# Kernel tuning notes

Measured on AMD Instinct MI355X. Metric: run time of the kernel, lower is better.

Reference implementation:

```python
import jax, jax.numpy as jnp
import numpy as np

B, N, D, H = 4, 2048, 512, 8
HEAD = D // H
TEMP = 8.0


def setup_inputs() -> dict:
    key = jax.random.key(0)
    k1, k2, k3, k4 = jax.random.split(key, 4)
    return {
        "keys": jax.random.normal(k1, (B, N, D), dtype=jnp.float32),
        "queries": jax.random.normal(k2, (B, N, D), dtype=jnp.float32),
        "values": jax.random.normal(k3, (B, N, D), dtype=jnp.float32),
        "W_comb": jax.random.normal(k4, (D, D), dtype=jnp.float32) * (1.0 / np.sqrt(D)),
        "b_comb": jnp.zeros((D,), dtype=jnp.float32),
    }


def reference(keys, queries, values, W_comb, b_comb):
    b, nk, d = keys.shape
    nq = queries.shape[1]
    h, hd = H, HEAD
    # split heads: (b, n, d) -> (b, n, h, hd)
    k = keys.reshape(b, nk, h, hd)
    q = queries.reshape(b, nq, h, hd)
    v = values.reshape(b, nk, h, hd)
    # scaled dot-product attention per head
    logits = jnp.einsum("bqhd,bkhd->bhqk", q, k) / TEMP  # (b, h, nq, nk)
    w = jax.nn.softmax(logits, axis=-1)
    out = jnp.einsum("bhqk,bkhd->bqhd", w, v).reshape(b, nq, d)
    # head_combine: Linear with bias (torch: x @ W.T + b)
    return out @ W_comb.T + b_comb
```

## Files before the change

kernel.cpp:

```cpp
#include <hip/hip_runtime.h>

#define B_ 4
#define N_ 2048
#define D_ 512
#define H_ 8

typedef __attribute__((ext_vector_type(8))) short bf16x8;
typedef __attribute__((ext_vector_type(4))) short bf16x4;
typedef __attribute__((ext_vector_type(4))) float f32x4;

#define KP 68

__device__ __forceinline__ unsigned short f32_to_bf16(float f) {
  unsigned int u = __float_as_uint(f);
  u += 0x7FFFu + ((u >> 16) & 1u);
  return (unsigned short)(u >> 16);
}

__device__ __forceinline__ unsigned int pack2_bf16(float a, float b) {
  return (unsigned int)f32_to_bf16(a) | ((unsigned int)f32_to_bf16(b) << 16);
}

__device__ __forceinline__ bf16x8 cvt8_bf16(float4 a, float4 b, float s) {
  union { unsigned int u[4]; bf16x8 v; } r;
  r.u[0] = pack2_bf16(a.x * s, a.y * s);
  r.u[1] = pack2_bf16(a.z * s, a.w * s);
  r.u[2] = pack2_bf16(b.x * s, b.y * s);
  r.u[3] = pack2_bf16(b.z * s, b.w * s);
  return r.v;
}

__device__ __forceinline__ float fast_exp2(float x) {
#if __has_builtin(__builtin_amdgcn_exp2f)
  return __builtin_amdgcn_exp2f(x);
#else
  return exp2f(x);
#endif
}

__device__ __forceinline__ f32x4 mfma16(bf16x4 a, bf16x4 b, f32x4 c) {
#if __has_builtin(__builtin_amdgcn_mfma_f32_16x16x16_bf16)
  return __builtin_amdgcn_mfma_f32_16x16x16_bf16(a, b, c, 0, 0, 0);
#else
  return __builtin_amdgcn_mfma_f32_16x16x16bf16_1k(a, b, c, 0, 0, 0);
#endif
}

__global__ __launch_bounds__(256) void convert_kernel(
    const float* __restrict__ Kf, const float* __restrict__ Vf,
    unsigned short* __restrict__ Kb, unsigned short* __restrict__ Vt) {
  __shared__ float tile[64 * 72];
  const int tid = threadIdx.x;
  if (blockIdx.x < 1024) {
    int gid = blockIdx.x * 256 + tid;
    const float4* K4 = (const float4*)Kf;
    for (int i = gid; i < (B_ * N_ * D_) / 4; i += 262144) {
      float4 k = K4[i];
      ((uint2*)Kb)[i] = make_uint2(pack2_bf16(k.x, k.y), pack2_bf16(k.z, k.w));
    }
  } else {
    int bid = blockIdx.x - 1024;
    int nt = bid & 31, bh = bid >> 5;
    int b = bh >> 3, h = bh & 7;
    int n0 = nt * 64;
#pragma unroll
    for (int i = 0; i < 4; ++i) {
      int idx = i * 256 + tid;
      int r = idx >> 4, c = idx & 15;
      *(float4*)&tile[r * 72 + c * 4] =
          *(const float4*)(Vf + (size_t)(b * N_ + n0 + r) * D_ + h * 64 + c * 4);
    }
    __syncthreads();
    int d = tid >> 2, c = tid & 3;
    unsigned int o[8];
#pragma unroll
    for (int j = 0; j < 8; ++j)
      o[j] = pack2_bf16(tile[(c * 16 + 2 * j) * 72 + d],
                        tile[(c * 16 + 2 * j + 1) * 72 + d]);
    unsigned short* dst = Vt + ((size_t)bh * 64 + d) * N_ + n0 + c * 16;
    *(bf16x8*)dst = *(bf16x8*)&o[0];
    *(bf16x8*)(dst + 8) = *(bf16x8*)&o[4];
  }
}

__global__ __launch_bounds__(256, 2) void attn_kernel(
    const float* __restrict__ Qf, const unsigned short* __restrict__ Kb,
    const unsigned short* __restrict__ Vt, unsigned short* __restrict__ Ob) {
  __shared__ unsigned short Kl[2][64 * KP];
  __shared__ unsigned short Vl[2][64 * KP];

  const int tid = threadIdx.x;
  const int w = tid >> 6;
  const int lane = tid & 63;
  const int lr = lane & 15;
  const int lq = lane >> 4;

  const int lid = blockIdx.y * gridDim.x + blockIdx.x;
  const int xcd = lid & 7;
  const int lin = lid >> 3;
  const int bh = xcd * 4 + (lin >> 4);
  const int qb = (lin & 15) * 128;

  const size_t slab = (size_t)(bh >> 3) * N_ * D_ + (size_t)(bh & 7) * 64;
  const unsigned short* kbase = Kb + slab;
  const unsigned short* vtbase = Vt + (size_t)bh * 64 * N_;

  bf16x8 qa[2][2];
  {
    const float qs = 0.125f * 1.4426950408889634f;
#pragma unroll
    for (int g = 0; g < 2; ++g) {
      const float* qrow =
          Qf + slab + (size_t)(qb + w * 32 + g * 16 + lr) * D_;
      float4 a0 = *(const float4*)(qrow + 8 * lq);
      float4 a1 = *(const float4*)(qrow + 8 * lq + 4);
      qa[g][0] = cvt8_bf16(a0, a1, qs);
      float4 b0 = *(const float4*)(qrow + 32 + 8 * lq);
      float4 b1 = *(const float4*)(qrow + 36 + 8 * lq);
      qa[g][1] = cvt8_bf16(b0, b1, qs);
    }
  }

  f32x4 O[4][2];
#pragma unroll
  for (int i = 0; i < 4; ++i)
#pragma unroll
    for (int g = 0; g < 2; ++g) O[i][g] = (f32x4){0.f, 0.f, 0.f, 0.f};
  float l_g[2] = {0.f, 0.f};

  const int st_r = tid >> 3;
  const int st_c = tid & 7;

  {
    const unsigned short* ksrc = kbase + (size_t)st_r * D_ + st_c * 8;
    bf16x8 a = *(const bf16x8*)ksrc;
    bf16x8 b = *(const bf16x8*)(ksrc + (size_t)32 * D_);
    const unsigned short* vsrc = vtbase + (size_t)st_r * N_ + st_c * 8;
    bf16x8 c = *(const bf16x8*)vsrc;
    bf16x8 d = *(const bf16x8*)(vsrc + (size_t)32 * N_);
    *(bf16x8*)&Kl[0][st_r * KP + st_c * 8] = a;
    *(bf16x8*)&Kl[0][(st_r + 32) * KP + st_c * 8] = b;
    *(bf16x8*)&Vl[0][st_r * KP + st_c * 8] = c;
    *(bf16x8*)&Vl[0][(st_r + 32) * KP + st_c * 8] = d;
  }

  for (int kt = 0; kt < 32; ++kt) {
    const int p = kt & 1;
    __syncthreads();

    bf16x8 nk0, nk1, nv0, nv1;
    const bool more = (kt + 1) < 32;
    if (more) {
      const int kb1 = (kt + 1) * 64;
      const unsigned short* ksrc = kbase + (size_t)(kb1 + st_r) * D_ + st_c * 8;
      nk0 = *(const bf16x8*)ksrc;
      nk1 = *(const bf16x8*)(ksrc + (size_t)32 * D_);
      const unsigned short* vsrc = vtbase + (size_t)st_r * N_ + kb1 + st_c * 8;
      nv0 = *(const bf16x8*)vsrc;
      nv1 = *(const bf16x8*)(vsrc + (size_t)32 * N_);
    }

    f32x4 S[4][2];
#pragma unroll
    for (int nt = 0; nt < 4; ++nt) {
      bf16x8 kf0 = *(const bf16x8*)&Kl[p][(nt * 16 + lr) * KP + 8 * lq];
      bf16x8 kf1 = *(const bf16x8*)&Kl[p][(nt * 16 + lr) * KP + 32 + 8 * lq];
#pragma unroll
      for (int g = 0; g < 2; ++g) {
        S[nt][g] = __builtin_amdgcn_mfma_f32_16x16x32_bf16(
            kf0, qa[g][0], (f32x4){0.f, 0.f, 0.f, 0.f}, 0, 0, 0);
        S[nt][g] = __builtin_amdgcn_mfma_f32_16x16x32_bf16(kf1, qa[g][1],
                                                           S[nt][g], 0, 0, 0);
      }
    }

    bf16x4 pf[4][2];
#pragma unroll
    for (int nt = 0; nt < 4; ++nt)
#pragma unroll
      for (int g = 0; g < 2; ++g) {
        float p0 = fast_exp2(S[nt][g][0]);
        float p1 = fast_exp2(S[nt][g][1]);
        float p2 = fast_exp2(S[nt][g][2]);
        float p3 = fast_exp2(S[nt][g][3]);
        l_g[g] += (p0 + p1) + (p2 + p3);
        uint2 packed = make_uint2(pack2_bf16(p0, p1), pack2_bf16(p2, p3));
        pf[nt][g] = *(bf16x4*)&packed;
      }

#pragma unroll
    for (int dt = 0; dt < 4; ++dt) {
#pragma unroll
      for (int nt = 0; nt < 4; ++nt) {
        bf16x4 vf =
            *(const bf16x4*)&Vl[p][(dt * 16 + lr) * KP + nt * 16 + 4 * lq];
#pragma unroll
        for (int g = 0; g < 2; ++g)
          O[dt][g] = mfma16(vf, pf[nt][g], O[dt][g]);
      }
    }

    if (more) {
      *(bf16x8*)&Kl[1 - p][st_r * KP + st_c * 8] = nk0;
      *(bf16x8*)&Kl[1 - p][(st_r + 32) * KP + st_c * 8] = nk1;
      *(bf16x8*)&Vl[1 - p][st_r * KP + st_c * 8] = nv0;
      *(bf16x8*)&Vl[1 - p][(st_r + 32) * KP + st_c * 8] = nv1;
    }
  }

#pragma unroll
  for (int g = 0; g < 2; ++g) {
    l_g[g] += __shfl_xor(l_g[g], 16);
    l_g[g] += __shfl_xor(l_g[g], 32);
  }

  __syncthreads();
  unsigned short* SR = &Kl[0][0];
#pragma unroll
  for (int g = 0; g < 2; ++g) {
    float linv = 1.0f / l_g[g];
#pragma unroll
    for (int dt = 0; dt < 4; ++dt) {
      float v0 = O[dt][g][0] * linv;
      float v1 = O[dt][g][1] * linv;
      float v2 = O[dt][g][2] * linv;
      float v3 = O[dt][g][3] * linv;
      uint2 packed = make_uint2(pack2_bf16(v0, v1), pack2_bf16(v2, v3));
      *(bf16x4*)&SR[(w * 32 + g * 16 + lr) * KP + dt * 16 + lq * 4] =
          *(bf16x4*)&packed;
    }
  }
  __syncthreads();
  {
    const int row = tid >> 1, half = tid & 1;
    unsigned short* dst = Ob + slab + (size_t)(qb + row) * D_ + half * 32;
    const unsigned short* src = &SR[row * KP + half * 32];
    *(bf16x8*)dst = *(const bf16x8*)src;
    *(bf16x8*)(dst + 8) = *(const bf16x8*)(src + 8);
    *(bf16x8*)(dst + 16) = *(const bf16x8*)(src + 16);
    *(bf16x8*)(dst + 24) = *(const bf16x8*)(src + 24);
  }
}

#define GP 68
__global__ __launch_bounds__(256, 2) void gemm_kernel(
    const unsigned short* __restrict__ A, const float* __restrict__ Wf,
    const float* __restrict__ bias, float* __restrict__ out) {
  __shared__ unsigned short A_lds[2][64 * GP];
  __shared__ unsigned short W_lds[2][128 * GP];

  const int tid = threadIdx.x;
  const int w = tid >> 6;
  const int lane = tid & 63;
  const int lr = lane & 15;
  const int lq = lane >> 4;

  const int bid = blockIdx.x;
  const int xcd = bid & 7;
  const int lin = bid >> 3;
  const int mb = (xcd * 16 + (lin >> 2)) * 64;
  const int cb = (lin & 3) * 128;

  const int dc = (tid & 7) * 8;
  const int r0 = tid >> 3;

  f32x4 acc[8];
#pragma unroll
  for (int i = 0; i < 8; ++i) acc[i] = (f32x4){0.f, 0.f, 0.f, 0.f};

  {
    *(bf16x8*)&A_lds[0][r0 * GP + dc] =
        *(const bf16x8*)(A + (size_t)(mb + r0) * D_ + dc);
    *(bf16x8*)&A_lds[0][(r0 + 32) * GP + dc] =
        *(const bf16x8*)(A + (size_t)(mb + r0 + 32) * D_ + dc);
#pragma unroll
    for (int j = 0; j < 4; ++j) {
      const float* wsrc = Wf + (size_t)(cb + r0 + 32 * j) * D_ + dc;
      float4 wa = *(const float4*)wsrc;
      float4 wb = *(const float4*)(wsrc + 4);
      *(bf16x8*)&W_lds[0][(r0 + 32 * j) * GP + dc] = cvt8_bf16(wa, wb, 1.0f);
    }
  }

  for (int kt = 0; kt < 8; ++kt) {
    const int p = kt & 1;
    __syncthreads();

    bf16x8 na0, na1;
    float4 nwA[4], nwB[4];
    const bool more = (kt + 1) < 8;
    if (more) {
      const int k1 = (kt + 1) * 64;
      na0 = *(const bf16x8*)(A + (size_t)(mb + r0) * D_ + k1 + dc);
      na1 = *(const bf16x8*)(A + (size_t)(mb + r0 + 32) * D_ + k1 + dc);
#pragma unroll
      for (int j = 0; j < 4; ++j) {
        const float* wsrc = Wf + (size_t)(cb + r0 + 32 * j) * D_ + k1 + dc;
        nwA[j] = *(const float4*)wsrc;
        nwB[j] = *(const float4*)(wsrc + 4);
      }
    }

    bf16x8 a0 = *(const bf16x8*)&A_lds[p][(w * 16 + lr) * GP + 8 * lq];
    bf16x8 a1 = *(const bf16x8*)&A_lds[p][(w * 16 + lr) * GP + 32 + 8 * lq];
#pragma unroll
    for (int nt = 0; nt < 8; ++nt) {
      bf16x8 b0 = *(const bf16x8*)&W_lds[p][(nt * 16 + lr) * GP + 8 * lq];
      bf16x8 b1 = *(const bf16x8*)&W_lds[p][(nt * 16 + lr) * GP + 32 + 8 * lq];
      acc[nt] = __builtin_amdgcn_mfma_f32_16x16x32_bf16(a0, b0, acc[nt], 0, 0, 0);
      acc[nt] = __builtin_amdgcn_mfma_f32_16x16x32_bf16(a1, b1, acc[nt], 0, 0, 0);
    }

    if (more) {
      *(bf16x8*)&A_lds[1 - p][r0 * GP + dc] = na0;
      *(bf16x8*)&A_lds[1 - p][(r0 + 32) * GP + dc] = na1;
#pragma unroll
      for (int j = 0; j < 4; ++j)
        *(bf16x8*)&W_lds[1 - p][(r0 + 32 * j) * GP + dc] =
            cvt8_bf16(nwA[j], nwB[j], 1.0f);
    }
  }

#pragma unroll
  for (int nt = 0; nt < 8; ++nt) {
    float bc = bias[cb + nt * 16 + lr];
#pragma unroll
    for (int rr = 0; rr < 4; ++rr) {
      int row = mb + w * 16 + lq * 4 + rr;
      out[(size_t)row * D_ + cb + nt * 16 + lr] = acc[nt][rr] + bc;
    }
  }
}

extern "C" void kernel_launch(void* const* d_in, const int* in_sizes, int n_in,
                              void* d_out, int out_size, void* d_ws,
                              size_t ws_size, hipStream_t stream) {
  (void)in_sizes; (void)n_in; (void)out_size; (void)ws_size;
  const float* keys    = (const float*)d_in[0];
  const float* queries = (const float*)d_in[1];
  const float* values  = (const float*)d_in[2];
  const float* W       = (const float*)d_in[3];
  const float* bias    = (const float*)d_in[4];
  float* out = (float*)d_out;

  char* ws = (char*)d_ws;
  unsigned short* Kb = (unsigned short*)(ws + 8388608);
  unsigned short* Vt = (unsigned short*)(ws + 16777216);
  unsigned short* Ab = (unsigned short*)(ws + 25690112);

  convert_kernel<<<2048, 256, 0, stream>>>(keys, values, Kb, Vt);

  attn_kernel<<<dim3(N_ / 128, B_ * H_), 256, 0, stream>>>(queries, Kb, Vt, Ab);

  gemm_kernel<<<512, 256, 0, stream>>>(Ab, W, bias, out);
}
```

Baseline: 163.7 us.

## Fuse convert, attention and projection into one persistent kernel with grid barriers

Merges the three separate launches (K/V bf16 conversion, attention, head-combine GEMM) into a single 512-block kernel that separates the phases with software grid-wide barriers built on atomic counters, which are reset by a memset before each launch. The aim is to remove the launch gaps and tail effects between kernels. In exchange it adds a memset, atomic spin-wait barriers, and the requirement that all 512 blocks be co-resident. Fewer blocks now do the convert phase than before.

```diff
diff --git a/kernel.cpp b/kernel.cpp
--- a/kernel.cpp
+++ b/kernel.cpp
@@ -4,12 +4,14 @@
 #define N_ 2048
 #define D_ 512
 #define H_ 8
+#define NBLK 512
 
 typedef __attribute__((ext_vector_type(8))) short bf16x8;
 typedef __attribute__((ext_vector_type(4))) short bf16x4;
 typedef __attribute__((ext_vector_type(4))) float f32x4;
 
 #define KP 68
+#define GP 68
 
 __device__ __forceinline__ unsigned short f32_to_bf16(float f) {
   unsigned int u = __float_as_uint(f);
@@ -46,288 +48,324 @@
 #endif
 }
 
-__global__ __launch_bounds__(256) void convert_kernel(
-    const float* __restrict__ Kf, const float* __restrict__ Vf,
-    unsigned short* __restrict__ Kb, unsigned short* __restrict__ Vt) {
-  __shared__ float tile[64 * 72];
-  const int tid = threadIdx.x;
-  if (blockIdx.x < 1024) {
-    int gid = blockIdx.x * 256 + tid;
-    const float4* K4 = (const float4*)Kf;
-    for (int i = gid; i < (B_ * N_ * D_) / 4; i += 262144) {
-      float4 k = K4[i];
-      ((uint2*)Kb)[i] = make_uint2(pack2_bf16(k.x, k.y), pack2_bf16(k.z, k.w));
-    }
-  } else {
-    int bid = blockIdx.x - 1024;
-    int nt = bid & 31, bh = bid >> 5;
-    int b = bh >> 3, h = bh & 7;
-    int n0 = nt * 64;
-#pragma unroll
-    for (int i = 0; i < 4; ++i) {
-      int idx = i * 256 + tid;
-      int r = idx >> 4, c = idx & 15;
-      *(float4*)&tile[r * 72 + c * 4] =
-          *(const float4*)(Vf + (size_t)(b * N_ + n0 + r) * D_ + h * 64 + c * 4);
-    }
-    __syncthreads();
-    int d = tid >> 2, c = tid & 3;
-    unsigned int o[8];
-#pragma unroll
-    for (int j = 0; j < 8; ++j)
-      o[j] = pack2_bf16(tile[(c * 16 + 2 * j) * 72 + d],
-                        tile[(c * 16 + 2 * j + 1) * 72 + d]);
-    unsigned short* dst = Vt + ((size_t)bh * 64 + d) * N_ + n0 + c * 16;
-    *(bf16x8*)dst = *(bf16x8*)&o[0];
-    *(bf16x8*)(dst + 8) = *(bf16x8*)&o[4];
-  }
-}
-
-__global__ __launch_bounds__(256, 2) void attn_kernel(
-    const float* __restrict__ Qf, const unsigned short* __restrict__ Kb,
-    const unsigned short* __restrict__ Vt, unsigned short* __restrict__ Ob) {
-  __shared__ unsigned short Kl[2][64 * KP];
-  __shared__ unsigned short Vl[2][64 * KP];
-
-  const int tid = threadIdx.x;
-  const int w = tid >> 6;
-  const int lane = tid & 63;
-  const int lr = lane & 15;
-  const int lq = lane >> 4;
-
-  const int lid = blockIdx.y * gridDim.x + blockIdx.x;
-  const int xcd = lid & 7;
-  const int lin = lid >> 3;
-  const int bh = xcd * 4 + (lin >> 4);
-  const int qb = (lin & 15) * 128;
-
-  const size_t slab = (size_t)(bh >> 3) * N_ * D_ + (size_t)(bh & 7) * 64;
-  const unsigned short* kbase = Kb + slab;
-  const unsigned short* vtbase = Vt + (size_t)bh * 64 * N_;
-
-  bf16x8 qa[2][2];
-  {
-    const float qs = 0.125f * 1.4426950408889634f;
-#pragma unroll
-    for (int g = 0; g < 2; ++g) {
-      const float* qrow =
-          Qf + slab + (size_t)(qb + w * 32 + g * 16 + lr) * D_;
-      float4 a0 = *(const float4*)(qrow + 8 * lq);
-      float4 a1 = *(const float4*)(qrow + 8 * lq + 4);
-      qa[g][0] = cvt8_bf16(a0, a1, qs);
-      float4 b0 = *(const float4*)(qrow + 32 + 8 * lq);
-      float4 b1 = *(const float4*)(qrow + 36 + 8 * lq);
-      qa[g][1] = cvt8_bf16(b0, b1, qs);
-    }
-  }
-
-  f32x4 O[4][2];
-#pragma unroll
-  for (int i = 0; i < 4; ++i)
-#pragma unroll
-    for (int g = 0; g < 2; ++g) O[i][g] = (f32x4){0.f, 0.f, 0.f, 0.f};
-  float l_g[2] = {0.f, 0.f};
-
-  const int st_r = tid >> 3;
-  const int st_c = tid & 7;
-
-  {
-    const unsigned short* ksrc = kbase + (size_t)st_r * D_ + st_c * 8;
-    bf16x8 a = *(const bf16x8*)ksrc;
-    bf16x8 b = *(const bf16x8*)(ksrc + (size_t)32 * D_);
-    const unsigned short* vsrc = vtbase + (size_t)st_r * N_ + st_c * 8;
-    bf16x8 c = *(const bf16x8*)vsrc;
-    bf16x8 d = *(const bf16x8*)(vsrc + (size_t)32 * N_);
-    *(bf16x8*)&Kl[0][st_r * KP + st_c * 8] = a;
-    *(bf16x8*)&Kl[0][(st_r + 32) * KP + st_c * 8] = b;
-    *(bf16x8*)&Vl[0][st_r * KP + st_c * 8] = c;
-    *(bf16x8*)&Vl[0][(st_r + 32) * KP + st_c * 8] = d;
-  }
-
-  for (int kt = 0; kt < 32; ++kt) {
-    const int p = kt & 1;
-    __syncthreads();
-
-    bf16x8 nk0, nk1, nv0, nv1;
-    const bool more = (kt + 1) < 32;
-    if (more) {
-      const int kb1 = (kt + 1) * 64;
-      const unsigned short* ksrc = kbase + (size_t)(kb1 + st_r) * D_ + st_c * 8;
-      nk0 = *(const bf16x8*)ksrc;
-      nk1 = *(const bf16x8*)(ksrc + (size_t)32 * D_);
-      const unsigned short* vsrc = vtbase + (size_t)st_r * N_ + kb1 + st_c * 8;
-      nv0 = *(const bf16x8*)vsrc;
-      nv1 = *(const bf16x8*)(vsrc + (size_t)32 * N_);
-    }
-
-    f32x4 S[4][2];
-#pragma unroll
-    for (int nt = 0; nt < 4; ++nt) {
-      bf16x8 kf0 = *(const bf16x8*)&Kl[p][(nt * 16 + lr) * KP + 8 * lq];
-      bf16x8 kf1 = *(const bf16x8*)&Kl[p][(nt * 16 + lr) * KP + 32 + 8 * lq];
-#pragma unroll
-      for (int g = 0; g < 2; ++g) {
-        S[nt][g] = __builtin_amdgcn_mfma_f32_16x16x32_bf16(
-            kf0, qa[g][0], (f32x4){0.f, 0.f, 0.f, 0.f}, 0, 0, 0);
-        S[nt][g] = __builtin_amdgcn_mfma_f32_16x16x32_bf16(kf1, qa[g][1],
-                                                           S[nt][g], 0, 0, 0);
-      }
-    }
-
-    bf16x4 pf[4][2];
-#pragma unroll
-    for (int nt = 0; nt < 4; ++nt)
-#pragma unroll
-      for (int g = 0; g < 2; ++g) {
-        float p0 = fast_exp2(S[nt][g][0]);
-        float p1 = fast_exp2(S[nt][g][1]);
-        float p2 = fast_exp2(S[nt][g][2]);
-        float p3 = fast_exp2(S[nt][g][3]);
-        l_g[g] += (p0 + p1) + (p2 + p3);
-        uint2 packed = make_uint2(pack2_bf16(p0, p1), pack2_bf16(p2, p3));
-        pf[nt][g] = *(bf16x4*)&packed;
-      }
-
-#pragma unroll
-    for (int dt = 0; dt < 4; ++dt) {
-#pragma unroll
-      for (int nt = 0; nt < 4; ++nt) {
-        bf16x4 vf =
-            *(const bf16x4*)&Vl[p][(dt * 16 + lr) * KP + nt * 16 + 4 * lq];
-#pragma unroll
-        for (int g = 0; g < 2; ++g)
-          O[dt][g] = mfma16(vf, pf[nt][g], O[dt][g]);
-      }
-    }
-
-    if (more) {
-      *(bf16x8*)&Kl[1 - p][st_r * KP + st_c * 8] = nk0;
-      *(bf16x8*)&Kl[1 - p][(st_r + 32) * KP + st_c * 8] = nk1;
-      *(bf16x8*)&Vl[1 - p][st_r * KP + st_c * 8] = nv0;
-      *(bf16x8*)&Vl[1 - p][(st_r + 32) * KP + st_c * 8] = nv1;
-    }
-  }
-
-#pragma unroll
-  for (int g = 0; g < 2; ++g) {
-    l_g[g] += __shfl_xor(l_g[g], 16);
-    l_g[g] += __shfl_xor(l_g[g], 32);
-  }
-
+__device__ __forceinline__ void grid_barrier(unsigned int* cnt,
+                                             unsigned int target) {
   __syncthreads();
-  unsigned short* SR = &Kl[0][0];
-#pragma unroll
-  for (int g = 0; g < 2; ++g) {
-    float linv = 1.0f / l_g[g];
-#pragma unroll
-    for (int dt = 0; dt < 4; ++dt) {
-      float v0 = O[dt][g][0] * linv;
-      float v1 = O[dt][g][1] * linv;
-      float v2 = O[dt][g][2] * linv;
-      float v3 = O[dt][g][3] * linv;
-      uint2 packed = make_uint2(pack2_bf16(v0, v1), pack2_bf16(v2, v3));
-      *(bf16x4*)&SR[(w * 32 + g * 16 + lr) * KP + dt * 16 + lq * 4] =
-          *(bf16x4*)&packed;
+  if (threadIdx.x == 0) {
+    __threadfence();
+    unsigned int v = __hip_atomic_fetch_add(cnt, 1u, __ATOMIC_ACQ_REL,
+                                            __HIP_MEMORY_SCOPE_AGENT) + 1u;
+    if (v < target) {
+      do {
+        __builtin_amdgcn_s_sleep(8);
+      } while (__hip_atomic_load(cnt, __ATOMIC_ACQUIRE,
+                                 __HIP_MEMORY_SCOPE_AGENT) < target);
     }
   }
   __syncthreads();
+}
+
+__global__ __launch_bounds__(256, 2) void fused_kernel(
+    const float* __restrict__ Kf, const float* __restrict__ Qf,
+    const float* __restrict__ Vf, const float* __restrict__ Wf,
+    const float* __restrict__ bias, unsigned short* __restrict__ Kb,
+    unsigned short* __restrict__ Vt, unsigned short* __restrict__ Ab,
+    float* __restrict__ out, unsigned int* __restrict__ cnt) {
+  __shared__ __align__(16) unsigned char smem_raw[52224];
+  const int tid = threadIdx.x;
+
   {
-    const int row = tid >> 1, half = tid & 1;
-    unsigned short* dst = Ob + slab + (size_t)(qb + row) * D_ + half * 32;
-    const unsigned short* src = &SR[row * KP + half * 32];
-    *(bf16x8*)dst = *(const bf16x8*)src;
-    *(bf16x8*)(dst + 8) = *(const bf16x8*)(src + 8);
-    *(bf16x8*)(dst + 16) = *(const bf16x8*)(src + 16);
-    *(bf16x8*)(dst + 24) = *(const bf16x8*)(src + 24);
+    float* tile = (float*)smem_raw;
+    {
+      int gid = blockIdx.x * 256 + tid;
+      const float4* K4 = (const float4*)Kf;
+      for (int i = gid; i < (B_ * N_ * D_) / 4; i += NBLK * 256) {
+        float4 k = K4[i];
+        ((uint2*)Kb)[i] =
+            make_uint2(pack2_bf16(k.x, k.y), pack2_bf16(k.z, k.w));
+      }
+    }
+#pragma unroll
+    for (int t2 = 0; t2 < 2; ++t2) {
+      const int t = blockIdx.x * 2 + t2;
+      const int nt = t & 31, bh = t >> 5;
+      const int b = bh >> 3, h = bh & 7;
+      const int n0 = nt * 64;
+      __syncthreads();
+#pragma unroll
+      for (int i = 0; i < 4; ++i) {
+        int idx = i * 256 + tid;
+        int r = idx >> 4, c = idx & 15;
+        *(float4*)&tile[r * 72 + c * 4] = *(const float4*)(
+            Vf + (size_t)(b * N_ + n0 + r) * D_ + h * 64 + c * 4);
+      }
+      __syncthreads();
+      int d = tid >> 2, c = tid & 3;
+      unsigned int o[8];
+#pragma unroll
+      for (int j = 0; j < 8; ++j)
+        o[j] = pack2_bf16(tile[(c * 16 + 2 * j) * 72 + d],
+                          tile[(c * 16 + 2 * j + 1) * 72 + d]);
+      unsigned short* dst = Vt + ((size_t)bh * 64 + d) * N_ + n0 + c * 16;
+      *(bf16x8*)dst = *(bf16x8*)&o[0];
+      *(bf16x8*)(dst + 8) = *(bf16x8*)&o[4];
+    }
   }
-}
-
-#define GP 68
-__global__ __launch_bounds__(256, 2) void gemm_kernel(
-    const unsigned short* __restrict__ A, const float* __restrict__ Wf,
-    const float* __restrict__ bias, float* __restrict__ out) {
-  __shared__ unsigned short A_lds[2][64 * GP];
-  __shared__ unsigned short W_lds[2][128 * GP];
-
-  const int tid = threadIdx.x;
-  const int w = tid >> 6;
-  const int lane = tid & 63;
-  const int lr = lane & 15;
-  const int lq = lane >> 4;
-
-  const int bid = blockIdx.x;
-  const int xcd = bid & 7;
-  const int lin = bid >> 3;
-  const int mb = (xcd * 16 + (lin >> 2)) * 64;
-  const int cb = (lin & 3) * 128;
-
-  const int dc = (tid & 7) * 8;
-  const int r0 = tid >> 3;
-
-  f32x4 acc[8];
-#pragma unroll
-  for (int i = 0; i < 8; ++i) acc[i] = (f32x4){0.f, 0.f, 0.f, 0.f};
+
+  grid_barrier(cnt, NBLK);
 
   {
-    *(bf16x8*)&A_lds[0][r0 * GP + dc] =
-        *(const bf16x8*)(A + (size_t)(mb + r0) * D_ + dc);
-    *(bf16x8*)&A_lds[0][(r0 + 32) * GP + dc] =
-        *(const bf16x8*)(A + (size_t)(mb + r0 + 32) * D_ + dc);
-#pragma unroll
-    for (int j = 0; j < 4; ++j) {
-      const float* wsrc = Wf + (size_t)(cb + r0 + 32 * j) * D_ + dc;
-      float4 wa = *(const float4*)wsrc;
-      float4 wb = *(const float4*)(wsrc + 4);
-      *(bf16x8*)&W_lds[0][(r0 + 32 * j) * GP + dc] = cvt8_bf16(wa, wb, 1.0f);
+    unsigned short* Kl = (unsigned short*)smem_raw;
+    unsigned short* Vl = (unsigned short*)smem_raw + 8704;
+
+    const int w = tid >> 6;
+    const int lane = tid & 63;
+    const int lr = lane & 15;
+    const int lq = lane >> 4;
+
+    const int lid = blockIdx.x;
+    const int xcd = lid & 7;
+    const int lin = lid >> 3;
+    const int bh = xcd * 4 + (lin >> 4);
+    const int qb = (lin & 15) * 128;
+
+    const size_t slab = (size_t)(bh >> 3) * N_ * D_ + (size_t)(bh & 7) * 64;
+    const unsigned short* kbase = Kb + slab;
+    const unsigned short* vtbase = Vt + (size_t)bh * 64 * N_;
+
+    bf16x8 qa[2][2];
+    {
+      const float qs = 0.125f * 1.4426950408889634f;
+#pragma unroll
+      for (int g = 0; g < 2; ++g) {
+        const float* qrow =
+            Qf + slab + (size_t)(qb + w * 32 + g * 16 + lr) * D_;
+        float4 a0 = *(const float4*)(qrow + 8 * lq);
+        float4 a1 = *(const float4*)(qrow + 8 * lq + 4);
+        qa[g][0] = cvt8_bf16(a0, a1, qs);
+        float4 b0 = *(const float4*)(qrow + 32 + 8 * lq);
+        float4 b1 = *(const float4*)(qrow + 36 + 8 * lq);
+        qa[g][1] = cvt8_bf16(b0, b1, qs);
+      }
+    }
+
+    f32x4 O[4][2];
+#pragma unroll
+    for (int i = 0; i < 4; ++i)
+#pragma unroll
+      for (int g = 0; g < 2; ++g) O[i][g] = (f32x4){0.f, 0.f, 0.f, 0.f};
+    float l_g[2] = {0.f, 0.f};
+
+    const int st_r = tid >> 3;
+    const int st_c = tid & 7;
+
+    {
+      const unsigned short* ksrc = kbase + (size_t)st_r * D_ + st_c * 8;
+      bf16x8 a = *(const bf16x8*)ksrc;
+      bf16x8 b = *(const bf16x8*)(ksrc + (size_t)32 * D_);
+      const unsigned short* vsrc = vtbase + (size_t)st_r * N_ + st_c * 8;
+      bf16x8 c = *(const bf16x8*)vsrc;
+      bf16x8 d = *(const bf16x8*)(vsrc + (size_t)32 * N_);
+      *(bf16x8*)&Kl[st_r * KP + st_c * 8] = a;
+      *(bf16x8*)&Kl[(st_r + 32) * KP + st_c * 8] = b;
+      *(bf16x8*)&Vl[st_r * KP + st_c * 8] = c;
+      *(bf16x8*)&Vl[(st_r + 32) * KP + st_c * 8] = d;
+    }
+
+    for (int kt = 0; kt < 32; ++kt) {
+      const int pb = (kt & 1) * 4352;
+      const int nb = 4352 - pb;
+      __syncthreads();
+
+      bf16x8 nk0, nk1, nv0, nv1;
+      const bool more = (kt + 1) < 32;
+      if (more) {
+        const int kb1 = (kt + 1) * 64;
+        const unsigned short* ksrc =
+            kbase + (size_t)(kb1 + st_r) * D_ + st_c * 8;
+        nk0 = *(const bf16x8*)ksrc;
+        nk1 = *(const bf16x8*)(ksrc + (size_t)32 * D_);
+        const unsigned short* vsrc =
+            vtbase + (size_t)st_r * N_ + kb1 + st_c * 8;
+        nv0 = *(const bf16x8*)vsrc;
+        nv1 = *(const bf16x8*)(vsrc + (size_t)32 * N_);
+      }
+
+      f32x4 S[4][2];
+#pragma unroll
+      for (int nt = 0; nt < 4; ++nt) {
+        bf16x8 kf0 = *(const bf16x8*)&Kl[pb + (nt * 16 + lr) * KP + 8 * lq];
+        bf16x8 kf1 =
+            *(const bf16x8*)&Kl[pb + (nt * 16 + lr) * KP + 32 + 8 * lq];
+#pragma unroll
+        for (int g = 0; g < 2; ++g) {
+          S[nt][g] = __builtin_amdgcn_mfma_f32_16x16x32_bf16(
+              kf0, qa[g][0], (f32x4){0.f, 0.f, 0.f, 0.f}, 0, 0, 0);
+          S[nt][g] = __builtin_amdgcn_mfma_f32_16x16x32_bf16(
+              kf1, qa[g][1], S[nt][g], 0, 0, 0);
+        }
+      }
+
+      bf16x4 pf[4][2];
+#pragma unroll
+      for (int nt = 0; nt < 4; ++nt)
+#pragma unroll
+        for (int g = 0; g < 2; ++g) {
+          float p0 = fast_exp2(S[nt][g][0]);
+          float p1 = fast_exp2(S[nt][g][1]);
+          float p2 = fast_exp2(S[nt][g][2]);
+          float p3 = fast_exp2(S[nt][g][3]);
+          l_g[g] += (p0 + p1) + (p2 + p3);
+          uint2 packed = make_uint2(pack2_bf16(p0, p1), pack2_bf16(p2, p3));
+          pf[nt][g] = *(bf16x4*)&packed;
+        }
+
+#pragma unroll
+      for (int dt = 0; dt < 4; ++dt) {
+#pragma unroll
+        for (int nt = 0; nt < 4; ++nt) {
+          bf16x4 vf = *(const bf16x4*)&Vl[pb + (dt * 16 + lr) * KP +
+                                          nt * 16 + 4 * lq];
+#pragma unroll
+          for (int g = 0; g < 2; ++g)
+            O[dt][g] = mfma16(vf, pf[nt][g], O[dt][g]);
+        }
+      }
+
+      if (more) {
+        *(bf16x8*)&Kl[nb + st_r * KP + st_c * 8] = nk0;
+        *(bf16x8*)&Kl[nb + (st_r + 32) * KP + st_c * 8] = nk1;
+        *(bf16x8*)&Vl[nb + st_r * KP + st_c * 8] = nv0;
+        *(bf16x8*)&Vl[nb + (st_r + 32) * KP + st_c * 8] = nv1;
+      }
+    }
+
+#pragma unroll
+    for (int g = 0; g < 2; ++g) {
+      l_g[g] += __shfl_xor(l_g[g], 16);
+      l_g[g] += __shfl_xor(l_g[g], 32);
+    }
+
+    __syncthreads();
+    unsigned short* SR = Kl;
+#pragma unroll
+    for (int g = 0; g < 2; ++g) {
+      float linv = 1.0f / l_g[g];
+#pragma unroll
+      for (int dt = 0; dt < 4; ++dt) {
+        float v0 = O[dt][g][0] * linv;
+        float v1 = O[dt][g][1] * linv;
+        float v2 = O[dt][g][2] * linv;
+        float v3 = O[dt][g][3] * linv;
+        uint2 packed = make_uint2(pack2_bf16(v0, v1), pack2_bf16(v2, v3));
+        *(bf16x4*)&SR[(w * 32 + g * 16 + lr) * KP + dt * 16 + lq * 4] =
+            *(bf16x4*)&packed;
+      }
+    }
+    __syncthreads();
+    {
+      const int row = tid >> 1, half = tid & 1;
+      unsigned short* dst = Ab + slab + (size_t)(qb + row) * D_ + half * 32;
+      const unsigned short* src = &SR[row * KP + half * 32];
+      *(bf16x8*)dst = *(const bf16x8*)src;
+      *(bf16x8*)(dst + 8) = *(const bf16x8*)(src + 8);
+      *(bf16x8*)(dst + 16) = *(const bf16x8*)(src + 16);
+      *(bf16x8*)(dst + 24) = *(const bf16x8*)(src + 24);
     }
   }
 
-  for (int kt = 0; kt < 8; ++kt) {
-    const int p = kt & 1;
-    __syncthreads();
-
-    bf16x8 na0, na1;
-    float4 nwA[4], nwB[4];
-    const bool more = (kt + 1) < 8;
-    if (more) {
-      const int k1 = (kt + 1) * 64;
-      na0 = *(const bf16x8*)(A + (size_t)(mb + r0) * D_ + k1 + dc);
-      na1 = *(const bf16x8*)(A + (size_t)(mb + r0 + 32) * D_ + k1 + dc);
+  grid_barrier(cnt + 1, NBLK);
+
+  {
+    unsigned short* A_lds = (unsigned short*)smem_raw;
+    unsigned short* W_lds = (unsigned short*)smem_raw + 8704;
+
+    const int w = tid >> 6;
+    const int lane = tid & 63;
+    const int lr = lane & 15;
+    const int lq = lane >> 4;
+
+    const int bid = blockIdx.x;
+    const int xcd = bid & 7;
+    const int lin = bid >> 3;
+    const int mb = (xcd * 16 + (lin >> 2)) * 64;
+    const int cb = (lin & 3) * 128;
+
+    const int dc = (tid & 7) * 8;
+    const int r0 = tid >> 3;
+
+    f32x4 acc[8];
+#pragma unroll
+    for (int i = 0; i < 8; ++i) acc[i] = (f32x4){0.f, 0.f, 0.f, 0.f};
+
+    {
+      *(bf16x8*)&A_lds[r0 * GP + dc] =
+          *(const bf16x8*)(Ab + (size_t)(mb + r0) * D_ + dc);
+      *(bf16x8*)&A_lds[(r0 + 32) * GP + dc] =
+          *(const bf16x8*)(Ab + (size_t)(mb + r0 + 32) * D_ + dc);
 #pragma unroll
       for (int j = 0; j < 4; ++j) {
-        const float* wsrc = Wf + (size_t)(cb + r0 + 32 * j) * D_ + k1 + dc;
-        nwA[j] = *(const float4*)wsrc;
-        nwB[j] = *(const float4*)(wsrc + 4);
-      }
-    }
-
-    bf16x8 a0 = *(const bf16x8*)&A_lds[p][(w * 16 + lr) * GP + 8 * lq];
-    bf16x8 a1 = *(const bf16x8*)&A_lds[p][(w * 16 + lr) * GP + 32 + 8 * lq];
+        const float* wsrc = Wf + (size_t)(cb + r0 + 32 * j) * D_ + dc;
+        float4 wa = *(const float4*)wsrc;
+        float4 wb = *(const float4*)(wsrc + 4);
+        *(bf16x8*)&W_lds[(r0 + 32 * j) * GP + dc] = cvt8_bf16(wa, wb, 1.0f);
+      }
+    }
+
+    for (int kt = 0; kt < 8; ++kt) {
+      const int pa = (kt & 1) * 4352;
+      const int pw = (kt & 1) * 8704;
+      const int na = 4352 - pa;
+      const int nw = 8704 - pw;
+      __syncthreads();
+
+      bf16x8 na0, na1;
+      float4 nwA[4], nwB[4];
+      const bool more = (kt + 1) < 8;
+      if (more) {
+        const int k1 = (kt + 1) * 64;
+        na0 = *(const bf16x8*)(Ab + (size_t)(mb + r0) * D_ + k1 + dc);
+        na1 = *(const bf16x8*)(Ab + (size_t)(mb + r0 + 32) * D_ + k1 + dc);
+#pragma unroll
+        for (int j = 0; j < 4; ++j) {
+          const float* wsrc = Wf + (size_t)(cb + r0 + 32 * j) * D_ + k1 + dc;
+          nwA[j] = *(const float4*)wsrc;
+          nwB[j] = *(const float4*)(wsrc + 4);
+        }
+      }
+
+      bf16x8 a0 = *(const bf16x8*)&A_lds[pa + (w * 16 + lr) * GP + 8 * lq];
+      bf16x8 a1 =
+          *(const bf16x8*)&A_lds[pa + (w * 16 + lr) * GP + 32 + 8 * lq];
+#pragma unroll
+      for (int nt = 0; nt < 8; ++nt) {
+        bf16x8 b0 = *(const bf16x8*)&W_lds[pw + (nt * 16 + lr) * GP + 8 * lq];
+        bf16x8 b1 =
+            *(const bf16x8*)&W_lds[pw + (nt * 16 + lr) * GP + 32 + 8 * lq];
+        acc[nt] =
+            __builtin_amdgcn_mfma_f32_16x16x32_bf16(a0, b0, acc[nt], 0, 0, 0);
+        acc[nt] =
+            __builtin_amdgcn_mfma_f32_16x16x32_bf16(a1, b1, acc[nt], 0, 0, 0);
+      }
+
+      if (more) {
+        *(bf16x8*)&A_lds[na + r0 * GP + dc] = na0;
+        *(bf16x8*)&A_lds[na + (r0 + 32) * GP + dc] = na1;
+#pragma unroll
+        for (int j = 0; j < 4; ++j)
+          *(bf16x8*)&W_lds[nw + (r0 + 32 * j) * GP + dc] =
+              cvt8_bf16(nwA[j], nwB[j], 1.0f);
+      }
+    }
+
 #pragma unroll
     for (int nt = 0; nt < 8; ++nt) {
-      bf16x8 b0 = *(const bf16x8*)&W_lds[p][(nt * 16 + lr) * GP + 8 * lq];
-      bf16x8 b1 = *(const bf16x8*)&W_lds[p][(nt * 16 + lr) * GP + 32 + 8 * lq];
-      acc[nt] = __builtin_amdgcn_mfma_f32_16x16x32_bf16(a0, b0, acc[nt], 0, 0, 0);
-      acc[nt] = __builtin_amdgcn_mfma_f32_16x16x32_bf16(a1, b1, acc[nt], 0, 0, 0);
-    }
-
-    if (more) {
-      *(bf16x8*)&A_lds[1 - p][r0 * GP + dc] = na0;
-      *(bf16x8*)&A_lds[1 - p][(r0 + 32) * GP + dc] = na1;
-#pragma unroll
-      for (int j = 0; j < 4; ++j)
-        *(bf16x8*)&W_lds[1 - p][(r0 + 32 * j) * GP + dc] =
-            cvt8_bf16(nwA[j], nwB[j], 1.0f);
-    }
-  }
-
-#pragma unroll
-  for (int nt = 0; nt < 8; ++nt) {
-    float bc = bias[cb + nt * 16 + lr];
-#pragma unroll
-    for (int rr = 0; rr < 4; ++rr) {
-      int row = mb + w * 16 + lq * 4 + rr;
-      out[(size_t)row * D_ + cb + nt * 16 + lr] = acc[nt][rr] + bc;
+      float bc = bias[cb + nt * 16 + lr];
+#pragma unroll
+      for (int rr = 0; rr < 4; ++rr) {
+        int row = mb + w * 16 + lq * 4 + rr;
+        out[(size_t)row * D_ + cb + nt * 16 + lr] = acc[nt][rr] + bc;
+      }
     }
   }
 }
@@ -347,10 +385,10 @@
   unsigned short* Kb = (unsigned short*)(ws + 8388608);
   unsigned short* Vt = (unsigned short*)(ws + 16777216);
   unsigned short* Ab = (unsigned short*)(ws + 25690112);
-
-  convert_kernel<<<2048, 256, 0, stream>>>(keys, values, Kb, Vt);
-
-  attn_kernel<<<dim3(N_ / 128, B_ * H_), 256, 0, stream>>>(queries, Kb, Vt, Ab);
-
-  gemm_kernel<<<512, 256, 0, stream>>>(Ab, W, bias, out);
-}
+  unsigned int* cnt  = (unsigned int*)(ws + 34078720);
+
+  hipMemsetAsync(cnt, 0, 8, stream);
+
+  fused_kernel<<<NBLK, 256, 0, stream>>>(keys, queries, values, W, bias,
+                                         Kb, Vt, Ab, out, cnt);
+}
```

After: 381.5 us. 2.33x slower.
